# Performance work log

Measured on AMD Instinct MI355X. Metric: run time of the kernel, lower is better.

The kernel has to match this reference:

```python
import jax, jax.numpy as jnp
import numpy as np

B = 65536
LAYERS = [256, 512, 512, 256]


def setup_inputs() -> dict:
    key = jax.random.key(0)
    ks = jax.random.split(key, 10)
    inp = {"data": jax.random.normal(ks[0], (B, LAYERS[0]), dtype=jnp.float32)}
    for i in range(3):
        n_in, n_out = LAYERS[i], LAYERS[i + 1]
        # link weights ~ U[0,1) like random.random(); bias params[0] zeroed in torch code
        inp[f"W{i+1}"] = jax.random.uniform(ks[1 + 3 * i], (n_in, n_out), dtype=jnp.float32)
        inp[f"b{i+1}"] = jnp.zeros((n_out,), dtype=jnp.float32)
        # per-node activation params a = params[1:6], torch.rand init
        inp[f"a{i+1}"] = jax.random.uniform(ks[2 + 3 * i], (n_out, 5), dtype=jnp.float32)
    return inp


def _act(x, a):
    # x: [B, n], a: [n, 5]; a0*tanh(x)*sin(a1*x+a2) + a3*x + a4  (per-node params broadcast over batch)
    return a[:, 0] * jnp.tanh(x) * jnp.sin(a[:, 1] * x + a[:, 2]) + a[:, 3] * x + a[:, 4]


def reference(data, W1, b1, a1, W2, b2, a2, W3, b3, a3):
    h = _act(data @ W1 + b1, a1)
    h = _act(h @ W2 + b2, a2)
    h = _act(h @ W3 + b3, a3)
    return jax.nn.softmax(h, axis=1)
```

## Files before the change

kernel.cpp:

```cpp
#include <hip/hip_runtime.h>

#define BATCH 65536

typedef float f32x4 __attribute__((ext_vector_type(4)));
typedef _Float16 f16x8 __attribute__((ext_vector_type(8)));

__device__ __forceinline__ void async_ld16(const void* g, void* l) {
  __builtin_amdgcn_global_load_lds(
      (const __attribute__((address_space(1))) void*)g,
      (__attribute__((address_space(3))) void*)l, 16, 0, 0);
}

__device__ __forceinline__ float act_f(float x, float a0, float a1, float a2,
                                       float a3, float a4) {
  float ax = fabsf(x);
  float e = __builtin_amdgcn_exp2f(ax * -2.8853900817779268f);
  float th = (1.0f - e) * __builtin_amdgcn_rcpf(1.0f + e);
  th = copysignf(th, x);
  float arg = fmaf(a1, x, a2);
  float rev = arg * 0.15915494309189535f;
  rev -= floorf(rev);
  float s = __builtin_amdgcn_sinf(rev);
  return fmaf(a3, x, fmaf(a0 * th, s, a4));
}

__global__ __launch_bounds__(256) void splitT_k(const float* __restrict__ W,
                                                _Float16* __restrict__ hi,
                                                _Float16* __restrict__ lo,
                                                int K, int N) {
  const int i = blockIdx.x * 256 + threadIdx.x;
  if (i >= K * N) return;
  const int k = i / N, n = i % N;
  const float w = W[i];
  const _Float16 h = (_Float16)w;
  hi[(size_t)n * K + k] = h;
  lo[(size_t)n * K + k] = (_Float16)(w - (float)h);
}

__device__ __forceinline__ f32x4 mfma3(f16x8 ah, f16x8 al, f16x8 bh, f16x8 bl,
                                       f32x4 c) {
  c = __builtin_amdgcn_mfma_f32_16x16x32_f16(ah, bh, c, 0, 0, 0);
  c = __builtin_amdgcn_mfma_f32_16x16x32_f16(ah, bl, c, 0, 0, 0);
  c = __builtin_amdgcn_mfma_f32_16x16x32_f16(al, bh, c, 0, 0, 0);
  return c;
}

template <bool AF32, bool FINAL>
__global__ __launch_bounds__(256, 2) void gemm_act(
    const float* __restrict__ Af, const _Float16* __restrict__ Ahi,
    const _Float16* __restrict__ Alo, const _Float16* __restrict__ Bhi,
    const _Float16* __restrict__ Blo, const float* __restrict__ bias,
    const float* __restrict__ ap, _Float16* __restrict__ Chi,
    _Float16* __restrict__ Clo, float* __restrict__ Cout, int K, int N) {
  __shared__ __align__(16) _Float16 sA[8192];
  __shared__ __align__(16) _Float16 sB[16384];

  const int tid = threadIdx.x;
  const int wv = tid >> 6;
  const int lane = tid & 63;
  const int wm = wv >> 1, wn = wv & 1;
  const int m16 = lane & 15, quad = lane >> 4;
  const int col0 = blockIdx.x * 256;
  const int row0 = blockIdx.y * 128;

  const int rl4 = lane >> 2, sl4 = lane & 3;
  const int sg4 = sl4 ^ ((rl4 >> 1) & 3);
  const int rl8 = lane >> 3, sl8 = lane & 7;
  const int sg8 = sl8 ^ rl8;
  const int fswz = (quad ^ ((m16 >> 1) & 3)) * 8;
  const int rc7 = m16 & 7;

  f32x4 acc[4][8];
  const f32x4 zero = {0.f, 0.f, 0.f, 0.f};
#pragma unroll
  for (int i = 0; i < 4; ++i)
#pragma unroll
    for (int j = 0; j < 8; ++j) acc[i][j] = zero;

  const int nk = K >> 5;
  for (int kt = 0; kt < nk; ++kt) {
    const int k0 = kt << 5;
    if (AF32) {
      float* sAf = (float*)sA;
#pragma unroll
      for (int t = 0; t < 4; ++t) {
        const int c = wv * 4 + t;
        const size_t ga = (size_t)(row0 + c * 8 + rl8) * K + k0 + sg8 * 4;
        async_ld16(Af + ga, (void*)&sAf[c * 256]);
      }
    } else {
#pragma unroll
      for (int t = 0; t < 2; ++t) {
        const int c = wv * 2 + t;
        const size_t ga = (size_t)(row0 + c * 16 + rl4) * K + k0 + sg4 * 8;
        async_ld16(Ahi + ga, (void*)&sA[c * 512]);
        async_ld16(Alo + ga, (void*)&sA[4096 + c * 512]);
      }
    }
#pragma unroll
    for (int t = 0; t < 4; ++t) {
      const int c = wv * 4 + t;
      const size_t gb = (size_t)(col0 + c * 16 + rl4) * K + k0 + sg4 * 8;
      async_ld16(Bhi + gb, (void*)&sB[c * 512]);
      async_ld16(Blo + gb, (void*)&sB[8192 + c * 512]);
    }
    __syncthreads();

    f16x8 ah[4], al[4];
#pragma unroll
    for (int tm = 0; tm < 4; ++tm) {
      if (AF32) {
        const int chunk = wm * 8 + tm * 2 + (m16 >> 3);
        const float* sAf = (const float*)sA + chunk * 256 + rc7 * 32;
        const f32x4 x0 = *(const f32x4*)(sAf + ((2 * quad) ^ rc7) * 4);
        const f32x4 x1 = *(const f32x4*)(sAf + ((2 * quad + 1) ^ rc7) * 4);
#pragma unroll
        for (int j = 0; j < 4; ++j) {
          const _Float16 h0 = (_Float16)x0[j];
          ah[tm][j] = h0;
          al[tm][j] = (_Float16)(x0[j] - (float)h0);
          const _Float16 h1 = (_Float16)x1[j];
          ah[tm][4 + j] = h1;
          al[tm][4 + j] = (_Float16)(x1[j] - (float)h1);
        }
      } else {
        const int idx = (wm * 4 + tm) * 512 + m16 * 32 + fswz;
        ah[tm] = *(const f16x8*)&sA[idx];
        al[tm] = *(const f16x8*)&sA[4096 + idx];
      }
    }
#pragma unroll
    for (int tn = 0; tn < 8; ++tn) {
      const int idx = (wn * 8 + tn) * 512 + m16 * 32 + fswz;
      const f16x8 bh = *(const f16x8*)&sB[idx];
      const f16x8 bl = *(const f16x8*)&sB[8192 + idx];
#pragma unroll
      for (int tm = 0; tm < 4; ++tm)
        acc[tm][tn] = mfma3(ah[tm], al[tm], bh, bl, acc[tm][tn]);
    }
    __syncthreads();
  }

  if (!FINAL) {
#pragma unroll
    for (int tn = 0; tn < 8; ++tn) {
      const int col = col0 + wn * 128 + tn * 16 + m16;
      const float bs = bias[col];
      const float p0 = ap[col * 5 + 0];
      const float p1 = ap[col * 5 + 1];
      const float p2 = ap[col * 5 + 2];
      const float p3 = ap[col * 5 + 3];
      const float p4 = ap[col * 5 + 4];
#pragma unroll
      for (int tm = 0; tm < 4; ++tm) {
        const int row = row0 + wm * 64 + tm * 16 + quad * 4;
#pragma unroll
        for (int r = 0; r < 4; ++r) {
          const float y = act_f(acc[tm][tn][r] + bs, p0, p1, p2, p3, p4);
          const size_t o = (size_t)(row + r) * N + col;
          const _Float16 h = (_Float16)y;
          Chi[o] = h;
          Clo[o] = (_Float16)(y - (float)h);
        }
      }
    }
  } else {
    const float L2E = 1.4426950408889634f;
    float mx[16], sm[16];
#pragma unroll
    for (int i = 0; i < 16; ++i) mx[i] = -1e30f;
#pragma unroll
    for (int tn = 0; tn < 8; ++tn) {
      const int col = wn * 128 + tn * 16 + m16;
      const float bs = bias[col];
      const float p0 = ap[col * 5 + 0];
      const float p1 = ap[col * 5 + 1];
      const float p2 = ap[col * 5 + 2];
      const float p3 = ap[col * 5 + 3];
      const float p4 = ap[col * 5 + 4];
#pragma unroll
      for (int tm = 0; tm < 4; ++tm)
#pragma unroll
        for (int r = 0; r < 4; ++r) {
          const float y = act_f(acc[tm][tn][r] + bs, p0, p1, p2, p3, p4);
          acc[tm][tn][r] = y;
          mx[tm * 4 + r] = fmaxf(mx[tm * 4 + r], y);
        }
    }
#pragma unroll
    for (int i = 0; i < 16; ++i)
#pragma unroll
      for (int off = 1; off < 16; off <<= 1)
        mx[i] = fmaxf(mx[i], __shfl_xor(mx[i], off));
#pragma unroll
    for (int i = 0; i < 16; ++i) sm[i] = 0.f;
#pragma unroll
    for (int tn = 0; tn < 8; ++tn)
#pragma unroll
      for (int tm = 0; tm < 4; ++tm)
#pragma unroll
        for (int r = 0; r < 4; ++r) {
          const float e = __builtin_amdgcn_exp2f(
              (acc[tm][tn][r] - mx[tm * 4 + r]) * L2E);
          acc[tm][tn][r] = e;
          sm[tm * 4 + r] += e;
        }
#pragma unroll
    for (int i = 0; i < 16; ++i)
#pragma unroll
      for (int off = 1; off < 16; off <<= 1) sm[i] += __shfl_xor(sm[i], off);
    float* part = (float*)sA;
    if (m16 == 0) {
#pragma unroll
      for (int tm = 0; tm < 4; ++tm)
#pragma unroll
        for (int r = 0; r < 4; ++r) {
          const int row = wm * 64 + tm * 16 + quad * 4 + r;
          part[(wn * 128 + row) * 2 + 0] = mx[tm * 4 + r];
          part[(wn * 128 + row) * 2 + 1] = sm[tm * 4 + r];
        }
    }
    __syncthreads();
    float sc[16];
#pragma unroll
    for (int tm = 0; tm < 4; ++tm)
#pragma unroll
      for (int r = 0; r < 4; ++r) {
        const int i = tm * 4 + r;
        const int row = wm * 64 + tm * 16 + quad * 4 + r;
        const float mo = part[((1 - wn) * 128 + row) * 2 + 0];
        const float so = part[((1 - wn) * 128 + row) * 2 + 1];
        const float M = fmaxf(mx[i], mo);
        const float a = __builtin_amdgcn_exp2f((mx[i] - M) * L2E);
        const float b = __builtin_amdgcn_exp2f((mo - M) * L2E);
        sc[i] = a * __builtin_amdgcn_rcpf(fmaf(sm[i], a, so * b));
      }
#pragma unroll
    for (int tn = 0; tn < 8; ++tn) {
      const int col = wn * 128 + tn * 16 + m16;
#pragma unroll
      for (int tm = 0; tm < 4; ++tm) {
        const int row = row0 + wm * 64 + tm * 16 + quad * 4;
#pragma unroll
        for (int r = 0; r < 4; ++r)
          Cout[(size_t)(row + r) * 256 + col] = acc[tm][tn][r] * sc[tm * 4 + r];
      }
    }
  }
}

extern "C" void kernel_launch(void* const* d_in, const int* in_sizes, int n_in,
                              void* d_out, int out_size, void* d_ws,
                              size_t ws_size, hipStream_t stream) {
  const float* data = (const float*)d_in[0];
  const float* W1 = (const float*)d_in[1];
  const float* b1 = (const float*)d_in[2];
  const float* a1 = (const float*)d_in[3];
  const float* W2 = (const float*)d_in[4];
  const float* b2 = (const float*)d_in[5];
  const float* a2 = (const float*)d_in[6];
  const float* W3 = (const float*)d_in[7];
  const float* b3 = (const float*)d_in[8];
  const float* a3 = (const float*)d_in[9];
  float* out = (float*)d_out;

  char* ws = (char*)d_ws;
  const size_t KB = 1024, MB = 1024 * 1024;
  _Float16* w1hi = (_Float16*)(ws + 0 * KB);
  _Float16* w1lo = (_Float16*)(ws + 256 * KB);
  _Float16* w2hi = (_Float16*)(ws + 512 * KB);
  _Float16* w2lo = (_Float16*)(ws + 1024 * KB);
  _Float16* w3hi = (_Float16*)(ws + 1536 * KB);
  _Float16* w3lo = (_Float16*)(ws + 1792 * KB);
  _Float16* h1hi = (_Float16*)(ws + 2 * MB);
  _Float16* h1lo = (_Float16*)(ws + 2 * MB + (size_t)BATCH * 512 * 2);
  _Float16* h2lo = (_Float16*)(ws + 2 * MB + (size_t)BATCH * 512 * 4);
  _Float16* h2hi = (_Float16*)d_out;

  splitT_k<<<(256 * 512 + 255) / 256, 256, 0, stream>>>(W1, w1hi, w1lo, 256, 512);
  splitT_k<<<(512 * 512 + 255) / 256, 256, 0, stream>>>(W2, w2hi, w2lo, 512, 512);
  splitT_k<<<(512 * 256 + 255) / 256, 256, 0, stream>>>(W3, w3hi, w3lo, 512, 256);

  gemm_act<true, false><<<dim3(2, BATCH / 128), 256, 0, stream>>>(
      data, nullptr, nullptr, w1hi, w1lo, b1, a1, h1hi, h1lo, nullptr, 256, 512);
  gemm_act<false, false><<<dim3(2, BATCH / 128), 256, 0, stream>>>(
      nullptr, h1hi, h1lo, w2hi, w2lo, b2, a2, h2hi, h2lo, nullptr, 512, 512);
  gemm_act<false, true><<<dim3(1, BATCH / 128), 256, 0, stream>>>(
      nullptr, h2hi, h2lo, w3hi, w3lo, b3, a3, nullptr, nullptr, out, 512, 256);
}
```

Measured before the change: 442.5 us.

## Template GEMM tiles, swap MFMA operands for row-contiguous stores, transpose activation params

Makes the fused GEMM+activation kernel templated on per-wave tile counts. Layers 1-2 now use 128x128 block tiles at 4 blocks per CU, and layer 3 uses 64x256 tiles. MFMA operands are swapped so each lane holds 4 consecutive columns of one row, which enables vectorized f16x4 and f32x4 stores and reduces the softmax row reductions to two shuffles. Bias and activation parameters are transposed by a small prep kernel so each lane reads them as float4 vectors. The smaller tiles reduce operand reuse and re-read the A operand more often, in exchange for higher occupancy and wider stores.

```diff
diff --git a/kernel.cpp b/kernel.cpp
--- a/kernel.cpp
+++ b/kernel.cpp
@@ -4,6 +4,7 @@
 
 typedef float f32x4 __attribute__((ext_vector_type(4)));
 typedef _Float16 f16x8 __attribute__((ext_vector_type(8)));
+typedef _Float16 f16x4 __attribute__((ext_vector_type(4)));
 
 __device__ __forceinline__ void async_ld16(const void* g, void* l) {
   __builtin_amdgcn_global_load_lds(
@@ -37,81 +38,95 @@
   lo[(size_t)n * K + k] = (_Float16)(w - (float)h);
 }
 
-__device__ __forceinline__ f32x4 mfma3(f16x8 ah, f16x8 al, f16x8 bh, f16x8 bl,
-                                       f32x4 c) {
-  c = __builtin_amdgcn_mfma_f32_16x16x32_f16(ah, bh, c, 0, 0, 0);
-  c = __builtin_amdgcn_mfma_f32_16x16x32_f16(ah, bl, c, 0, 0, 0);
-  c = __builtin_amdgcn_mfma_f32_16x16x32_f16(al, bh, c, 0, 0, 0);
+__global__ __launch_bounds__(256) void prep_params(const float* __restrict__ b,
+                                                   const float* __restrict__ a,
+                                                   float* __restrict__ Pt,
+                                                   int N) {
+  const int c = blockIdx.x * 256 + threadIdx.x;
+  if (c >= N) return;
+  Pt[c] = b[c];
+#pragma unroll
+  for (int j = 0; j < 5; ++j) Pt[(1 + j) * N + c] = a[c * 5 + j];
+}
+
+__device__ __forceinline__ f32x4 mfma3s(f16x8 wh, f16x8 wl, f16x8 xh,
+                                        f16x8 xl, f32x4 c) {
+  c = __builtin_amdgcn_mfma_f32_16x16x32_f16(wh, xh, c, 0, 0, 0);
+  c = __builtin_amdgcn_mfma_f32_16x16x32_f16(wh, xl, c, 0, 0, 0);
+  c = __builtin_amdgcn_mfma_f32_16x16x32_f16(wl, xh, c, 0, 0, 0);
   return c;
 }
 
-template <bool AF32, bool FINAL>
-__global__ __launch_bounds__(256, 2) void gemm_act(
+template <int MT, int NT, bool AF32, bool FINAL>
+__global__ __launch_bounds__(256, 4) void gemm_act(
     const float* __restrict__ Af, const _Float16* __restrict__ Ahi,
     const _Float16* __restrict__ Alo, const _Float16* __restrict__ Bhi,
-    const _Float16* __restrict__ Blo, const float* __restrict__ bias,
-    const float* __restrict__ ap, _Float16* __restrict__ Chi,
-    _Float16* __restrict__ Clo, float* __restrict__ Cout, int K, int N) {
-  __shared__ __align__(16) _Float16 sA[8192];
-  __shared__ __align__(16) _Float16 sB[16384];
+    const _Float16* __restrict__ Blo, const float* __restrict__ Pt,
+    _Float16* __restrict__ Chi, _Float16* __restrict__ Clo,
+    float* __restrict__ Cout, int K, int N) {
+  constexpr int MB_ = 2 * MT * 16;
+  constexpr int NB_ = 2 * NT * 16;
+  __shared__ __align__(16) _Float16 sA[MB_ * 64];
+  __shared__ __align__(16) _Float16 sB[NB_ * 64];
 
   const int tid = threadIdx.x;
-  const int wv = tid >> 6;
-  const int lane = tid & 63;
+  const int wv = tid >> 6, lane = tid & 63;
   const int wm = wv >> 1, wn = wv & 1;
   const int m16 = lane & 15, quad = lane >> 4;
-  const int col0 = blockIdx.x * 256;
-  const int row0 = blockIdx.y * 128;
-
-  const int rl4 = lane >> 2, sl4 = lane & 3;
-  const int sg4 = sl4 ^ ((rl4 >> 1) & 3);
-  const int rl8 = lane >> 3, sl8 = lane & 7;
-  const int sg8 = sl8 ^ rl8;
+  const int col0 = blockIdx.x * NB_;
+  const int row0 = blockIdx.y * MB_;
+  const int rl4 = lane >> 2, sg4 = (lane & 3) ^ ((rl4 >> 1) & 3);
+  const int rl8 = lane >> 3, sg8 = (lane & 7) ^ rl8;
   const int fswz = (quad ^ ((m16 >> 1) & 3)) * 8;
-  const int rc7 = m16 & 7;
-
-  f32x4 acc[4][8];
+
+  f32x4 acc[MT][NT];
   const f32x4 zero = {0.f, 0.f, 0.f, 0.f};
 #pragma unroll
-  for (int i = 0; i < 4; ++i)
-#pragma unroll
-    for (int j = 0; j < 8; ++j) acc[i][j] = zero;
+  for (int i = 0; i < MT; ++i)
+#pragma unroll
+    for (int j = 0; j < NT; ++j) acc[i][j] = zero;
 
   const int nk = K >> 5;
   for (int kt = 0; kt < nk; ++kt) {
     const int k0 = kt << 5;
-    if (AF32) {
+    if constexpr (AF32) {
       float* sAf = (float*)sA;
-#pragma unroll
-      for (int t = 0; t < 4; ++t) {
-        const int c = wv * 4 + t;
+      constexpr int PW = (MB_ / 8) / 4;
+#pragma unroll
+      for (int t = 0; t < PW; ++t) {
+        const int c = wv * PW + t;
         const size_t ga = (size_t)(row0 + c * 8 + rl8) * K + k0 + sg8 * 4;
         async_ld16(Af + ga, (void*)&sAf[c * 256]);
       }
     } else {
-#pragma unroll
-      for (int t = 0; t < 2; ++t) {
-        const int c = wv * 2 + t;
+      constexpr int PW = (MB_ / 16) / 4;
+#pragma unroll
+      for (int t = 0; t < PW; ++t) {
+        const int c = wv * PW + t;
         const size_t ga = (size_t)(row0 + c * 16 + rl4) * K + k0 + sg4 * 8;
         async_ld16(Ahi + ga, (void*)&sA[c * 512]);
-        async_ld16(Alo + ga, (void*)&sA[4096 + c * 512]);
-      }
-    }
-#pragma unroll
-    for (int t = 0; t < 4; ++t) {
-      const int c = wv * 4 + t;
-      const size_t gb = (size_t)(col0 + c * 16 + rl4) * K + k0 + sg4 * 8;
-      async_ld16(Bhi + gb, (void*)&sB[c * 512]);
-      async_ld16(Blo + gb, (void*)&sB[8192 + c * 512]);
+        async_ld16(Alo + ga, (void*)&sA[MB_ * 32 + c * 512]);
+      }
+    }
+    {
+      constexpr int PW = (NB_ / 16) / 4;
+#pragma unroll
+      for (int t = 0; t < PW; ++t) {
+        const int c = wv * PW + t;
+        const size_t gb = (size_t)(col0 + c * 16 + rl4) * K + k0 + sg4 * 8;
+        async_ld16(Bhi + gb, (void*)&sB[c * 512]);
+        async_ld16(Blo + gb, (void*)&sB[NB_ * 32 + c * 512]);
+      }
     }
     __syncthreads();
 
-    f16x8 ah[4], al[4];
-#pragma unroll
-    for (int tm = 0; tm < 4; ++tm) {
-      if (AF32) {
-        const int chunk = wm * 8 + tm * 2 + (m16 >> 3);
-        const float* sAf = (const float*)sA + chunk * 256 + rc7 * 32;
+    f16x8 ah[MT], al[MT];
+#pragma unroll
+    for (int tm = 0; tm < MT; ++tm) {
+      const int arow = wm * MT * 16 + tm * 16 + m16;
+      if constexpr (AF32) {
+        const float* sAf = (const float*)sA + arow * 32;
+        const int rc7 = m16 & 7;
         const f32x4 x0 = *(const f32x4*)(sAf + ((2 * quad) ^ rc7) * 4);
         const f32x4 x1 = *(const f32x4*)(sAf + ((2 * quad + 1) ^ rc7) * 4);
 #pragma unroll
@@ -124,126 +139,123 @@
           al[tm][4 + j] = (_Float16)(x1[j] - (float)h1);
         }
       } else {
-        const int idx = (wm * 4 + tm) * 512 + m16 * 32 + fswz;
+        const int idx = arow * 32 + fswz;
         ah[tm] = *(const f16x8*)&sA[idx];
-        al[tm] = *(const f16x8*)&sA[4096 + idx];
-      }
-    }
-#pragma unroll
-    for (int tn = 0; tn < 8; ++tn) {
-      const int idx = (wn * 8 + tn) * 512 + m16 * 32 + fswz;
+        al[tm] = *(const f16x8*)&sA[MB_ * 32 + idx];
+      }
+    }
+#pragma unroll
+    for (int tn = 0; tn < NT; ++tn) {
+      const int bcol = wn * NT * 16 + tn * 16 + m16;
+      const int idx = bcol * 32 + fswz;
       const f16x8 bh = *(const f16x8*)&sB[idx];
-      const f16x8 bl = *(const f16x8*)&sB[8192 + idx];
-#pragma unroll
-      for (int tm = 0; tm < 4; ++tm)
-        acc[tm][tn] = mfma3(ah[tm], al[tm], bh, bl, acc[tm][tn]);
+      const f16x8 bl = *(const f16x8*)&sB[NB_ * 32 + idx];
+#pragma unroll
+      for (int tm = 0; tm < MT; ++tm)
+        acc[tm][tn] = mfma3s(bh, bl, ah[tm], al[tm], acc[tm][tn]);
     }
     __syncthreads();
   }
 
-  if (!FINAL) {
-#pragma unroll
-    for (int tn = 0; tn < 8; ++tn) {
-      const int col = col0 + wn * 128 + tn * 16 + m16;
-      const float bs = bias[col];
-      const float p0 = ap[col * 5 + 0];
-      const float p1 = ap[col * 5 + 1];
-      const float p2 = ap[col * 5 + 2];
-      const float p3 = ap[col * 5 + 3];
-      const float p4 = ap[col * 5 + 4];
-#pragma unroll
-      for (int tm = 0; tm < 4; ++tm) {
-        const int row = row0 + wm * 64 + tm * 16 + quad * 4;
+  if constexpr (!FINAL) {
+#pragma unroll
+    for (int tn = 0; tn < NT; ++tn) {
+      const int colb = col0 + wn * NT * 16 + tn * 16 + quad * 4;
+      f32x4 P[6];
+#pragma unroll
+      for (int j = 0; j < 6; ++j) P[j] = *(const f32x4*)&Pt[j * N + colb];
+#pragma unroll
+      for (int tm = 0; tm < MT; ++tm) {
+        const int row = row0 + wm * MT * 16 + tm * 16 + m16;
+        f16x4 h4, l4;
 #pragma unroll
         for (int r = 0; r < 4; ++r) {
-          const float y = act_f(acc[tm][tn][r] + bs, p0, p1, p2, p3, p4);
-          const size_t o = (size_t)(row + r) * N + col;
+          const float y = act_f(acc[tm][tn][r] + P[0][r], P[1][r], P[2][r],
+                                P[3][r], P[4][r], P[5][r]);
           const _Float16 h = (_Float16)y;
-          Chi[o] = h;
-          Clo[o] = (_Float16)(y - (float)h);
+          h4[r] = h;
+          l4[r] = (_Float16)(y - (float)h);
         }
+        const size_t o = (size_t)row * N + colb;
+        *(f16x4*)&Chi[o] = h4;
+        *(f16x4*)&Clo[o] = l4;
       }
     }
   } else {
     const float L2E = 1.4426950408889634f;
-    float mx[16], sm[16];
-#pragma unroll
-    for (int i = 0; i < 16; ++i) mx[i] = -1e30f;
-#pragma unroll
-    for (int tn = 0; tn < 8; ++tn) {
-      const int col = wn * 128 + tn * 16 + m16;
-      const float bs = bias[col];
-      const float p0 = ap[col * 5 + 0];
-      const float p1 = ap[col * 5 + 1];
-      const float p2 = ap[col * 5 + 2];
-      const float p3 = ap[col * 5 + 3];
-      const float p4 = ap[col * 5 + 4];
-#pragma unroll
-      for (int tm = 0; tm < 4; ++tm)
+    float mx[MT], sm[MT];
+#pragma unroll
+    for (int tm = 0; tm < MT; ++tm) mx[tm] = -1e30f;
+#pragma unroll
+    for (int tn = 0; tn < NT; ++tn) {
+      const int colb = wn * NT * 16 + tn * 16 + quad * 4;
+      f32x4 P[6];
+#pragma unroll
+      for (int j = 0; j < 6; ++j) P[j] = *(const f32x4*)&Pt[j * N + colb];
+#pragma unroll
+      for (int tm = 0; tm < MT; ++tm)
 #pragma unroll
         for (int r = 0; r < 4; ++r) {
-          const float y = act_f(acc[tm][tn][r] + bs, p0, p1, p2, p3, p4);
+          const float y = act_f(acc[tm][tn][r] + P[0][r], P[1][r], P[2][r],
+                                P[3][r], P[4][r], P[5][r]);
           acc[tm][tn][r] = y;
-          mx[tm * 4 + r] = fmaxf(mx[tm * 4 + r], y);
+          mx[tm] = fmaxf(mx[tm], y);
         }
     }
 #pragma unroll
-    for (int i = 0; i < 16; ++i)
-#pragma unroll
-      for (int off = 1; off < 16; off <<= 1)
-        mx[i] = fmaxf(mx[i], __shfl_xor(mx[i], off));
-#pragma unroll
-    for (int i = 0; i < 16; ++i) sm[i] = 0.f;
-#pragma unroll
-    for (int tn = 0; tn < 8; ++tn)
-#pragma unroll
-      for (int tm = 0; tm < 4; ++tm)
+    for (int tm = 0; tm < MT; ++tm) {
+      mx[tm] = fmaxf(mx[tm], __shfl_xor(mx[tm], 16));
+      mx[tm] = fmaxf(mx[tm], __shfl_xor(mx[tm], 32));
+    }
+#pragma unroll
+    for (int tm = 0; tm < MT; ++tm) sm[tm] = 0.f;
+#pragma unroll
+    for (int tn = 0; tn < NT; ++tn)
+#pragma unroll
+      for (int tm = 0; tm < MT; ++tm)
 #pragma unroll
         for (int r = 0; r < 4; ++r) {
-          const float e = __builtin_amdgcn_exp2f(
-              (acc[tm][tn][r] - mx[tm * 4 + r]) * L2E);
+          const float e =
+              __builtin_amdgcn_exp2f((acc[tm][tn][r] - mx[tm]) * L2E);
           acc[tm][tn][r] = e;
-          sm[tm * 4 + r] += e;
+          sm[tm] += e;
         }
 #pragma unroll
-    for (int i = 0; i < 16; ++i)
-#pragma unroll
-      for (int off = 1; off < 16; off <<= 1) sm[i] += __shfl_xor(sm[i], off);
+    for (int tm = 0; tm < MT; ++tm) {
+      sm[tm] += __shfl_xor(sm[tm], 16);
+      sm[tm] += __shfl_xor(sm[tm], 32);
+    }
     float* part = (float*)sA;
-    if (m16 == 0) {
-#pragma unroll
-      for (int tm = 0; tm < 4; ++tm)
-#pragma unroll
-        for (int r = 0; r < 4; ++r) {
-          const int row = wm * 64 + tm * 16 + quad * 4 + r;
-          part[(wn * 128 + row) * 2 + 0] = mx[tm * 4 + r];
-          part[(wn * 128 + row) * 2 + 1] = sm[tm * 4 + r];
-        }
+    if (quad == 0) {
+#pragma unroll
+      for (int tm = 0; tm < MT; ++tm) {
+        const int rl = wm * MT * 16 + tm * 16 + m16;
+        part[(wn * MB_ + rl) * 2 + 0] = mx[tm];
+        part[(wn * MB_ + rl) * 2 + 1] = sm[tm];
+      }
     }
     __syncthreads();
-    float sc[16];
-#pragma unroll
-    for (int tm = 0; tm < 4; ++tm)
-#pragma unroll
-      for (int r = 0; r < 4; ++r) {
-        const int i = tm * 4 + r;
-        const int row = wm * 64 + tm * 16 + quad * 4 + r;
-        const float mo = part[((1 - wn) * 128 + row) * 2 + 0];
-        const float so = part[((1 - wn) * 128 + row) * 2 + 1];
-        const float M = fmaxf(mx[i], mo);
-        const float a = __builtin_amdgcn_exp2f((mx[i] - M) * L2E);
-        const float b = __builtin_amdgcn_exp2f((mo - M) * L2E);
-        sc[i] = a * __builtin_amdgcn_rcpf(fmaf(sm[i], a, so * b));
-      }
-#pragma unroll
-    for (int tn = 0; tn < 8; ++tn) {
-      const int col = wn * 128 + tn * 16 + m16;
-#pragma unroll
-      for (int tm = 0; tm < 4; ++tm) {
-        const int row = row0 + wm * 64 + tm * 16 + quad * 4;
-#pragma unroll
-        for (int r = 0; r < 4; ++r)
-          Cout[(size_t)(row + r) * 256 + col] = acc[tm][tn][r] * sc[tm * 4 + r];
+    float sc[MT];
+#pragma unroll
+    for (int tm = 0; tm < MT; ++tm) {
+      const int rl = wm * MT * 16 + tm * 16 + m16;
+      const float mo = part[((1 - wn) * MB_ + rl) * 2 + 0];
+      const float so = part[((1 - wn) * MB_ + rl) * 2 + 1];
+      const float M = fmaxf(mx[tm], mo);
+      const float a = __builtin_amdgcn_exp2f((mx[tm] - M) * L2E);
+      const float b = __builtin_amdgcn_exp2f((mo - M) * L2E);
+      sc[tm] = a * __builtin_amdgcn_rcpf(fmaf(sm[tm], a, so * b));
+    }
+#pragma unroll
+    for (int tn = 0; tn < NT; ++tn) {
+      const int colb = wn * NT * 16 + tn * 16 + quad * 4;
+#pragma unroll
+      for (int tm = 0; tm < MT; ++tm) {
+        const int row = row0 + wm * MT * 16 + tm * 16 + m16;
+        f32x4 v = acc[tm][tn];
+#pragma unroll
+        for (int r = 0; r < 4; ++r) v[r] *= sc[tm];
+        *(f32x4*)&Cout[(size_t)row * 256 + colb] = v;
       }
     }
   }
@@ -272,19 +284,25 @@
   _Float16* w2lo = (_Float16*)(ws + 1024 * KB);
   _Float16* w3hi = (_Float16*)(ws + 1536 * KB);
   _Float16* w3lo = (_Float16*)(ws + 1792 * KB);
-  _Float16* h1hi = (_Float16*)(ws + 2 * MB);
-  _Float16* h1lo = (_Float16*)(ws + 2 * MB + (size_t)BATCH * 512 * 2);
-  _Float16* h2lo = (_Float16*)(ws + 2 * MB + (size_t)BATCH * 512 * 4);
+  float* Pt1 = (float*)(ws + 2048 * KB);
+  float* Pt2 = (float*)(ws + 2064 * KB);
+  float* Pt3 = (float*)(ws + 2080 * KB);
+  _Float16* h1hi = (_Float16*)(ws + 2112 * KB);
+  _Float16* h1lo = (_Float16*)(ws + 2112 * KB + (size_t)BATCH * 512 * 2);
+  _Float16* h2lo = (_Float16*)(ws + 2112 * KB + (size_t)BATCH * 512 * 4);
   _Float16* h2hi = (_Float16*)d_out;
 
   splitT_k<<<(256 * 512 + 255) / 256, 256, 0, stream>>>(W1, w1hi, w1lo, 256, 512);
   splitT_k<<<(512 * 512 + 255) / 256, 256, 0, stream>>>(W2, w2hi, w2lo, 512, 512);
   splitT_k<<<(512 * 256 + 255) / 256, 256, 0, stream>>>(W3, w3hi, w3lo, 512, 256);
-
-  gemm_act<true, false><<<dim3(2, BATCH / 128), 256, 0, stream>>>(
-      data, nullptr, nullptr, w1hi, w1lo, b1, a1, h1hi, h1lo, nullptr, 256, 512);
-  gemm_act<false, false><<<dim3(2, BATCH / 128), 256, 0, stream>>>(
-      nullptr, h1hi, h1lo, w2hi, w2lo, b2, a2, h2hi, h2lo, nullptr, 512, 512);
-  gemm_act<false, true><<<dim3(1, BATCH / 128), 256, 0, stream>>>(
-      nullptr, h2hi, h2lo, w3hi, w3lo, b3, a3, nullptr, nullptr, out, 512, 256);
-}
+  prep_params<<<2, 256, 0, stream>>>(b1, a1, Pt1, 512);
+  prep_params<<<2, 256, 0, stream>>>(b2, a2, Pt2, 512);
+  prep_params<<<1, 256, 0, stream>>>(b3, a3, Pt3, 256);
+
+  gemm_act<4, 4, true, false><<<dim3(4, BATCH / 128), 256, 0, stream>>>(
+      data, nullptr, nullptr, w1hi, w1lo, Pt1, h1hi, h1lo, nullptr, 256, 512);
+  gemm_act<4, 4, false, false><<<dim3(4, BATCH / 128), 256, 0, stream>>>(
+      nullptr, h1hi, h1lo, w2hi, w2lo, Pt2, h2hi, h2lo, nullptr, 512, 512);
+  gemm_act<2, 8, false, true><<<dim3(1, BATCH / 64), 256, 0, stream>>>(
+      nullptr, h2hi, h2lo, w3hi, w3lo, Pt3, nullptr, nullptr, out, 512, 256);
+}
```

Measured after the change: 490.1 us. 10.8% more time.
